# Kernel optimization log

Hardware: AMD Instinct MI355X
Metric: run time of the kernel (lower is better)

The kernel has to match this reference:

```python
import jax, jax.numpy as jnp
import numpy as np
import math

D_MODEL = 64
D_STATE = 16
IMG = 64
GROUPS = 4
EPS = 1e-5


def group_norm(x, gamma, beta):
    B, C, H, W = x.shape
    xg = x.reshape(B, GROUPS, C // GROUPS, H, W)
    mu = xg.mean(axis=(2, 3, 4), keepdims=True)
    var = ((xg - mu) ** 2).mean(axis=(2, 3, 4), keepdims=True)
    xn = ((xg - mu) * jax.lax.rsqrt(var + EPS)).reshape(B, C, H, W)
    return xn * gamma[None, :, None, None] + beta[None, :, None, None]


def circ_conv(x, w, b=None):
    # 3x3 conv with circular padding, NCHW/OIHW
    xp = jnp.pad(x, ((0, 0), (0, 0), (1, 1), (1, 1)), mode='wrap')
    y = jax.lax.conv_general_dilated(xp, w, window_strides=(1, 1), padding='VALID',
                                     dimension_numbers=('NCHW', 'OIHW', 'NCHW'))
    if b is not None:
        y = y + b[None, :, None, None]
    return y


def setup_inputs() -> dict:
    key = jax.random.key(0)
    ks = jax.random.split(key, 6)
    B = 4
    u_t = jax.random.normal(ks[0], (B, D_MODEL, IMG, IMG), dtype=jnp.float32)
    s_prev = jax.random.normal(ks[1], (B, 3, D_MODEL, D_STATE, IMG, IMG), dtype=jnp.float32)
    gamma = jnp.ones((D_MODEL,), jnp.float32)
    beta = jnp.zeros((D_MODEL,), jnp.float32)
    w_delta = jax.random.normal(ks[2], (D_MODEL, D_MODEL, 3, 3), jnp.float32) * 0.05
    b_delta = jnp.zeros((D_MODEL,), jnp.float32)
    w_B = jax.random.normal(ks[3], (D_STATE, D_MODEL, 3, 3), jnp.float32) * 0.05
    w_C = jax.random.normal(ks[4], (D_STATE, D_MODEL, 3, 3), jnp.float32) * 0.05
    log_A_real = jnp.full((D_MODEL, D_STATE), math.log(0.5), jnp.float32)
    D_param = jnp.ones((D_MODEL,), jnp.float32)
    dt_inv_softplus = jnp.asarray(math.log(math.e - 1.0), jnp.float32)
    return {'u_t': u_t, 's_prev': s_prev, 'gamma': gamma, 'beta': beta,
            'w_delta': w_delta, 'b_delta': b_delta, 'w_B': w_B, 'w_C': w_C,
            'log_A_real': log_A_real, 'D_param': D_param, 'dt_inv_softplus': dt_inv_softplus}


def reference(u_t, s_prev, gamma, beta, w_delta, b_delta, w_B, w_C, log_A_real, D_param, dt_inv_softplus):
    B, D, H, W = u_t.shape
    N = D_STATE
    un = group_norm(u_t, gamma, beta)
    delta = jax.nn.softplus(circ_conv(un, w_delta, b_delta) + dt_inv_softplus)
    delta = jnp.clip(delta, 1e-4, 5.0)                     # [B,D,H,W]
    B_val = circ_conv(un, w_B)                              # [B,N,H,W]
    C_val = circ_conv(un, w_C)                              # [B,N,H,W]
    A = -jnp.exp(log_A_real)                                # [D,N]
    delta_bc = delta[:, :, None]                            # [B,D,1,H,W]
    A_bar = jnp.exp(delta_bc * A[None, :, :, None, None])   # [B,D,N,H,W]
    B_bar = delta_bc * B_val[:, None]                       # [B,D,N,H,W]
    m0, mx, my = s_prev[:, 0], s_prev[:, 1], s_prev[:, 2]   # each [B,D,N,H,W]
    # spectral gradient of m0 over last two (spatial) axes
    ky_ = np.fft.fftfreq(H).astype(np.float32) * 2.0 * np.pi
    kx_ = np.fft.fftfreq(W).astype(np.float32) * 2.0 * np.pi
    ky, kx = jnp.meshgrid(jnp.asarray(ky_), jnp.asarray(kx_), indexing='ij')
    m0f = jnp.fft.fft2(m0)
    grad_y = jnp.fft.ifft2(m0f * (1j * ky)).real
    grad_x = jnp.fft.ifft2(m0f * (1j * kx)).real
    m0_new = A_bar * m0 + B_bar * u_t[:, :, None]
    mx_new = A_bar * (mx - grad_x)
    my_new = A_bar * (my - grad_y)
    s_new = jnp.stack([m0_new, mx_new, my_new], axis=1)     # [B,3,D,N,H,W]
    y_state = jnp.einsum('bdnhw,bnhw->bdhw', m0_new, C_val)
    y_new = (y_state + u_t * D_param[None, :, None, None])[:, None]  # [B,1,D,H,W]
    return (y_new, s_new)
```

## Files before the change

### kernel.cpp

```cpp
#include <hip/hip_runtime.h>
#include <hip/hip_bf16.h>

#define B_ 4
#define D_ 64
#define N_ 16
#define HW_ 4096

#define LDSA 72
#define LDSB 66
#define EXPU 68

#define OFF_D2    0u
#define OFF_ATAB  8192u
#define OFF_MEAN  12288u
#define OFF_RSTD  12352u
#define OFF_W9    16384u
#define OFF_UNT   131072u
#define OFF_DELTA 2228224u
#define OFF_BVAL  6422528u
#define OFF_CVAL  7471104u
#define OFF_YBUF  8519680u

typedef __bf16 v8bf __attribute__((ext_vector_type(8)));
typedef float  v4f  __attribute__((ext_vector_type(4)));

__device__ __forceinline__ unsigned short f2bf(float f){
  __hip_bfloat16 h = __float2bfloat16(f);
  return *reinterpret_cast<unsigned short*>(&h);
}
__device__ __forceinline__ float bf2f(unsigned int u){
  union{unsigned int i; float f;} c; c.i = (u & 0xffffu)<<16; return c.f;
}
__device__ __forceinline__ v8bf ld8bf(const unsigned short* p){
  union{uint4 u; v8bf v;} c; c.u = *(const uint4*)p; return c.v;
}

__device__ __forceinline__ void bar_lgkm(){
  asm volatile("s_waitcnt lgkmcnt(0)" ::: "memory");
  __builtin_amdgcn_s_barrier();
  __builtin_amdgcn_sched_barrier(0);
}

__global__ void k_init(const float* __restrict__ logA,
                       unsigned short* __restrict__ D2w, float* __restrict__ Atab){
  int g = blockIdx.x*256 + threadIdx.x;
  if(g < 4096){
    int r = g>>6, m = g&63;
    int p = (r - m) & 63;
    float s = 0.f;
    for(int k=1;k<32;k++) s += (float)k * sinf(0.09817477042468103f * (float)(k*p));
    D2w[g] = f2bf(-0.0030679615757712823f * s);
  } else if(g < 5120){
    int idx = g - 4096;
    Atab[idx] = -__expf(logA[idx]);
  }
}

__global__ void k_wrepack(const float* __restrict__ wd,
                          const float* __restrict__ wB,
                          const float* __restrict__ wC,
                          unsigned short* __restrict__ W9){
  int idx = blockIdx.x*256 + threadIdx.x;
  if(idx >= 96*64) return;
  int co = idx>>6, ci = idx&63;
  const float* src;
  if(co < 64)      src = wd + ((size_t)co*64 + ci)*9;
  else if(co < 80) src = wB + ((size_t)(co-64)*64 + ci)*9;
  else             src = wC + ((size_t)(co-80)*64 + ci)*9;
  for(int tap=0; tap<9; tap++)
    W9[((size_t)tap*96 + co)*64 + ci] = f2bf(src[tap]);
}

__global__ void k_gnstats(const float* __restrict__ u,
                          float* __restrict__ meanw, float* __restrict__ rstdw){
  int bg = blockIdx.x;
  const float* base = u + (size_t)bg*65536;
  int t = threadIdx.x;
  float s=0.f, s2=0.f;
  for(int j=0;j<16;j++){
    float4 v = ((const float4*)base)[t + 1024*j];
    s  += v.x+v.y+v.z+v.w;
    s2 += v.x*v.x+v.y*v.y+v.z*v.z+v.w*v.w;
  }
  for(int o=32;o>0;o>>=1){ s += __shfl_down(s,o); s2 += __shfl_down(s2,o); }
  __shared__ float ls[16], ls2[16];
  int wv = t>>6;
  if((t&63)==0){ ls[wv]=s; ls2[wv]=s2; }
  __syncthreads();
  if(t==0){
    float S=0.f,S2=0.f;
    for(int i=0;i<16;i++){ S+=ls[i]; S2+=ls2[i]; }
    float mu = S/65536.f;
    float var = S2/65536.f - mu*mu;
    meanw[bg]=mu; rstdw[bg]=rsqrtf(var+1e-5f);
  }
}

__global__ __launch_bounds__(256) void k_unT(
    const float* __restrict__ u_t,
    const float* __restrict__ meanw, const float* __restrict__ rstdw,
    const float* __restrict__ gamma, const float* __restrict__ beta,
    unsigned short* __restrict__ unT){
  __shared__ unsigned short T[64*LDSA];
  int bid = blockIdx.x;
  int b = bid>>6, h = bid&63;
  int t = threadIdx.x;
  int w = t&63, cg = t>>6;
  #pragma unroll
  for(int i=0;i<16;i++){
    int c = cg*16 + i;
    float x = u_t[(((size_t)b*64 + c)*64 + h)*64 + w];
    int g = c>>4;
    float v = (x - meanw[b*4+g])*rstdw[b*4+g]*gamma[c] + beta[c];
    T[w*LDSA + c] = f2bf(v);
  }
  __syncthreads();
  int w2 = t>>2, cq = t&3;
  uint4 v0 = *(uint4*)&T[w2*LDSA + cq*16];
  uint4 v1 = *(uint4*)&T[w2*LDSA + cq*16 + 8];
  uint4* dst = (uint4*)(unT + ((size_t)b*HW_ + h*64 + w2)*64 + cq*16);
  dst[0] = v0; dst[1] = v1;
}

__global__ __launch_bounds__(256) void k_conv(
    const unsigned short* __restrict__ unT,
    const unsigned short* __restrict__ W9,
    const float* __restrict__ b_d,
    const float* __restrict__ dtp,
    float* __restrict__ deltaw, float* __restrict__ Bvalw, float* __restrict__ Cvalw){
  int bid = blockIdx.x;
  int b = bid>>6, h = bid&63;
  int t = threadIdx.x;
  int wv = t>>6, l = t&63;
  int lr = l&15, lk = l>>4;
  v4f acc[6];
  #pragma unroll
  for(int i=0;i<6;i++) acc[i] = (v4f){0.f,0.f,0.f,0.f};
  int wpix = wv*16 + lr;
  #pragma unroll
  for(int tap=0; tap<9; tap++){
    int dy = tap/3 - 1, dx = tap - (tap/3)*3 - 1;
    int hh = (h+dy)&63;
    int ww = (wpix+dx)&63;
    const unsigned short* bp = unT + ((size_t)b*HW_ + hh*64 + ww)*64;
    const unsigned short* ap = W9 + (size_t)tap*96*64;
    #pragma unroll
    for(int ks=0; ks<2; ks++){
      int k0 = ks*32 + lk*8;
      v8bf bfrag = ld8bf(bp + k0);
      #pragma unroll
      for(int mt=0; mt<6; mt++){
        v8bf afrag = ld8bf(ap + (mt*16+lr)*64 + k0);
        acc[mt] = __builtin_amdgcn_mfma_f32_16x16x32_bf16(afrag, bfrag, acc[mt], 0,0,0);
      }
    }
  }
  float dt = dtp[0];
  int p = h*64 + wpix;
  #pragma unroll
  for(int mt=0; mt<6; mt++){
    #pragma unroll
    for(int r=0;r<4;r++){
      int co = mt*16 + lk*4 + r;
      float v = acc[mt][r];
      if(co < 64){
        float x = v + b_d[co] + dt;
        float sp = (x > 15.f) ? x : log1pf(__expf(x));
        sp = fminf(fmaxf(sp, 1e-4f), 5.f);
        deltaw[((size_t)b*64 + co)*HW_ + p] = sp;
      } else if(co < 80){
        Bvalw[((size_t)b*16 + (co-64))*HW_ + p] = v;
      } else {
        Cvalw[((size_t)b*16 + (co-80))*HW_ + p] = v;
      }
    }
  }
}

__global__ __launch_bounds__(256, 4) void k_main(
    const float* __restrict__ u_t,
    const float* __restrict__ s_prev,
    const unsigned short* __restrict__ D2w,
    const float* __restrict__ Atab,
    const float* __restrict__ deltaw,
    const float* __restrict__ Bvalw,
    const float* __restrict__ Cvalw,
    float* __restrict__ ybuf,
    float* __restrict__ out_s){
  __shared__ __align__(16) unsigned short Mbuf[64*LDSA + 64*LDSB];
  __shared__ __align__(16) unsigned short D2s[64*LDSA];
  unsigned short* Ms72 = Mbuf;
  unsigned short* Ms66 = Mbuf + 64*LDSA;
  unsigned short* EXx  = Mbuf;
  unsigned short* EXy  = Mbuf + 64*EXPU;

  int bid = blockIdx.x;
  int pair = bid & 255;
  int b = pair & 3, d = pair >> 2;
  int nq = bid >> 8;
  int t = threadIdx.x;
  int wv = t>>6, l = t&63;
  int lr = l & 15, lk = l >> 4;
  int r0 = wv*16;

  size_t bd = (size_t)b*64 + d;
  const size_t PL = (size_t)D_*N_*HW_;
  size_t sbase = (size_t)b*3*PL + (size_t)d*N_*HW_;
  int n0 = nq*4;

  const float* m0base = s_prev + sbase;
  const float* mxbase = s_prev + sbase + PL;
  const float* mybase = s_prev + sbase + 2*PL;

  int g0 = t, g1 = t+256, g2 = t+512, g3 = t+768;

  uint4 d2v0 = ((const uint4*)D2w)[t];
  uint4 d2v1 = ((const uint4*)D2w)[t+256];
  { int r = t>>3, cb = t&7;            *(uint4*)&D2s[r*LDSA + cb*8] = d2v0; }
  { int c2 = t+256; int r = c2>>3, cb = c2&7; *(uint4*)&D2s[r*LDSA + cb*8] = d2v1; }
  const float4* uv4 = (const float4*)(u_t + bd*HW_);
  const float4* dv4 = (const float4*)(deltaw + bd*HW_);
  float4 uq0 = uv4[g0], uq1 = uv4[g1], uq2 = uv4[g2], uq3 = uv4[g3];
  float4 dq0 = dv4[g0], dq1 = dv4[g1], dq2 = dv4[g2], dq3 = dv4[g3];

  float4 yq0 = make_float4(0.f,0.f,0.f,0.f);
  float4 yq1 = yq0, yq2 = yq0, yq3 = yq0;

  for(int ni=0; ni<4; ni++){
    int n = n0 + ni;
    const float4* m0v = (const float4*)(m0base + (size_t)n*HW_);
    float4 pm0 = m0v[g0], pm1 = m0v[g1], pm2 = m0v[g2], pm3 = m0v[g3];
    const float4* mxv = (const float4*)(mxbase + (size_t)n*HW_);
    const float4* myv = (const float4*)(mybase + (size_t)n*HW_);
    float4 sx0 = mxv[g0], sx1 = mxv[g1], sx2 = mxv[g2], sx3 = mxv[g3];
    float4 sy0 = myv[g0], sy1 = myv[g1], sy2 = myv[g2], sy3 = myv[g3];

    #pragma unroll
    for(int j=0;j<4;j++){
      float4 v = (j==0)?pm0:(j==1)?pm1:(j==2)?pm2:pm3;
      int g = t + 256*j;
      int r = g>>4, cb = g&15;
      unsigned int lo = (unsigned int)f2bf(v.x) | ((unsigned int)f2bf(v.y)<<16);
      unsigned int hi = (unsigned int)f2bf(v.z) | ((unsigned int)f2bf(v.w)<<16);
      unsigned int* d72 = (unsigned int*)&Ms72[r*LDSA + cb*4];
      d72[0]=lo; d72[1]=hi;
      unsigned int* d66 = (unsigned int*)&Ms66[r*LDSB + cb*4];
      d66[0]=lo; d66[1]=hi;
    }
    bar_lgkm();

    v4f gxa[4], gya[4];
    #pragma unroll
    for(int ct=0; ct<4; ct++){
      v4f gx = {0.f,0.f,0.f,0.f}, gy = {0.f,0.f,0.f,0.f};
      #pragma unroll
      for(int ks=0; ks<2; ks++){
        int k0 = ks*32 + lk*8;
        v8bf a_gx = ld8bf(&D2s[(ct*16+lr)*LDSA + k0]);
        v8bf b_gx = ld8bf(&Ms72[(r0+lr)*LDSA + k0]);
        gx = __builtin_amdgcn_mfma_f32_16x16x32_bf16(a_gx, b_gx, gx, 0,0,0);
        union { unsigned short s[8]; v8bf v; } ag;
        #pragma unroll
        for(int i=0;i<8;i++) ag.s[i] = Ms66[(k0+i)*LDSB + ct*16 + lr];
        v8bf b_gy = ld8bf(&D2s[(r0+lr)*LDSA + k0]);
        gy = __builtin_amdgcn_mfma_f32_16x16x32_bf16(ag.v, b_gy, gy, 0,0,0);
      }
      gxa[ct] = gx; gya[ct] = gy;
    }
    bar_lgkm();

    #pragma unroll
    for(int ct=0; ct<4; ct++){
      int eo = (r0+lr)*EXPU + (ct*4+lk)*4;
      unsigned int x0 = (unsigned int)f2bf(gxa[ct][0]) | ((unsigned int)f2bf(gxa[ct][1])<<16);
      unsigned int x1 = (unsigned int)f2bf(gxa[ct][2]) | ((unsigned int)f2bf(gxa[ct][3])<<16);
      *(uint2*)&EXx[eo] = make_uint2(x0,x1);
      unsigned int y0 = (unsigned int)f2bf(gya[ct][0]) | ((unsigned int)f2bf(gya[ct][1])<<16);
      unsigned int y1 = (unsigned int)f2bf(gya[ct][2]) | ((unsigned int)f2bf(gya[ct][3])<<16);
      *(uint2*)&EXy[eo] = make_uint2(y0,y1);
    }
    bar_lgkm();

    float An = Atab[d*16 + n];
    const float4* Bv  = (const float4*)(Bvalw + ((size_t)b*16 + n)*HW_);
    const float4* Cv  = (const float4*)(Cvalw + ((size_t)b*16 + n)*HW_);
    float* so = out_s + sbase + (size_t)n*HW_;
    float4* so0 = (float4*)so;
    float4* so1 = (float4*)(so + PL);
    float4* so2 = (float4*)(so + 2*PL);

    #pragma unroll
    for(int k=0; k<4; k++){
      int g = t + 256*k;
      float4 B4  = Bv[g];
      float4 C4  = Cv[g];
      int eo = (g>>4)*EXPU + (g&15)*4;
      uint2 ux = *(const uint2*)&EXx[eo];
      uint2 uy = *(const uint2*)&EXy[eo];
      float4 m04 = (k==0)?pm0:(k==1)?pm1:(k==2)?pm2:pm3;
      float4 mx4 = (k==0)?sx0:(k==1)?sx1:(k==2)?sx2:sx3;
      float4 my4 = (k==0)?sy0:(k==1)?sy1:(k==2)?sy2:sy3;
      float4 u4  = (k==0)?uq0:(k==1)?uq1:(k==2)?uq2:uq3;
      float4 dv_ = (k==0)?dq0:(k==1)?dq1:(k==2)?dq2:dq3;
      float4 ab, m0n, mxn, myn;
      ab.x = __expf(dv_.x*An);
      ab.y = __expf(dv_.y*An);
      ab.z = __expf(dv_.z*An);
      ab.w = __expf(dv_.w*An);
      m0n.x = ab.x*m04.x + dv_.x*B4.x*u4.x;
      m0n.y = ab.y*m04.y + dv_.y*B4.y*u4.y;
      m0n.z = ab.z*m04.z + dv_.z*B4.z*u4.z;
      m0n.w = ab.w*m04.w + dv_.w*B4.w*u4.w;
      mxn.x = ab.x*(mx4.x - bf2f(ux.x));
      mxn.y = ab.y*(mx4.y - bf2f(ux.x>>16));
      mxn.z = ab.z*(mx4.z - bf2f(ux.y));
      mxn.w = ab.w*(mx4.w - bf2f(ux.y>>16));
      myn.x = ab.x*(my4.x - bf2f(uy.x));
      myn.y = ab.y*(my4.y - bf2f(uy.x>>16));
      myn.z = ab.z*(my4.z - bf2f(uy.y));
      myn.w = ab.w*(my4.w - bf2f(uy.y>>16));
      if(k==0){ yq0.x += m0n.x*C4.x; yq0.y += m0n.y*C4.y; yq0.z += m0n.z*C4.z; yq0.w += m0n.w*C4.w; }
      if(k==1){ yq1.x += m0n.x*C4.x; yq1.y += m0n.y*C4.y; yq1.z += m0n.z*C4.z; yq1.w += m0n.w*C4.w; }
      if(k==2){ yq2.x += m0n.x*C4.x; yq2.y += m0n.y*C4.y; yq2.z += m0n.z*C4.z; yq2.w += m0n.w*C4.w; }
      if(k==3){ yq3.x += m0n.x*C4.x; yq3.y += m0n.y*C4.y; yq3.z += m0n.z*C4.z; yq3.w += m0n.w*C4.w; }
      so0[g] = m0n;
      so1[g] = mxn;
      so2[g] = myn;
    }
    __syncthreads();
  }

  float* yb = ybuf + bd*HW_;
  #pragma unroll
  for(int k=0; k<4; k++){
    int p = 4*(t + 256*k);
    float4 yv = (k==0)?yq0:(k==1)?yq1:(k==2)?yq2:yq3;
    atomicAdd(&yb[p+0], yv.x);
    atomicAdd(&yb[p+1], yv.y);
    atomicAdd(&yb[p+2], yv.z);
    atomicAdd(&yb[p+3], yv.w);
  }
}

__global__ void k_y(const float* __restrict__ ybuf,
                    const float* __restrict__ u_t,
                    const float* __restrict__ Dp,
                    float* __restrict__ out_y){
  int i = blockIdx.x*blockDim.x + threadIdx.x;
  int d = (i>>10)&63;
  float Dv = Dp[d];
  float4 uv = ((const float4*)u_t)[i];
  float4 yv = ((const float4*)ybuf)[i];
  float4 o;
  o.x = yv.x + uv.x*Dv;
  o.y = yv.y + uv.y*Dv;
  o.z = yv.z + uv.z*Dv;
  o.w = yv.w + uv.w*Dv;
  ((float4*)out_y)[i] = o;
}

extern "C" void kernel_launch(void* const* d_in, const int* in_sizes, int n_in,
                              void* d_out, int out_size, void* d_ws, size_t ws_size,
                              hipStream_t stream){
  const float* u_t    = (const float*)d_in[0];
  const float* s_prev = (const float*)d_in[1];
  const float* gamma  = (const float*)d_in[2];
  const float* beta   = (const float*)d_in[3];
  const float* w_d    = (const float*)d_in[4];
  const float* b_d    = (const float*)d_in[5];
  const float* w_B    = (const float*)d_in[6];
  const float* w_C    = (const float*)d_in[7];
  const float* logA   = (const float*)d_in[8];
  const float* Dp     = (const float*)d_in[9];
  const float* dtp    = (const float*)d_in[10];

  char* ws = (char*)d_ws;
  unsigned short* D2w  = (unsigned short*)(ws + OFF_D2);
  float* Atab          = (float*)(ws + OFF_ATAB);
  float* meanw         = (float*)(ws + OFF_MEAN);
  float* rstdw         = (float*)(ws + OFF_RSTD);
  unsigned short* W9   = (unsigned short*)(ws + OFF_W9);
  unsigned short* unT  = (unsigned short*)(ws + OFF_UNT);
  float* deltaw        = (float*)(ws + OFF_DELTA);
  float* Bvalw         = (float*)(ws + OFF_BVAL);
  float* Cvalw         = (float*)(ws + OFF_CVAL);
  float* ybuf          = (float*)(ws + OFF_YBUF);

  float* out_y = (float*)d_out;
  float* out_s = out_y + 1048576;

  hipMemsetAsync(ws + OFF_YBUF, 0, 4u*1048576u, stream);
  k_init   <<<20, 256, 0, stream>>>(logA, D2w, Atab);
  k_wrepack<<<24, 256, 0, stream>>>(w_d, w_B, w_C, W9);
  k_gnstats<<<16, 1024, 0, stream>>>(u_t, meanw, rstdw);
  k_unT    <<<256, 256, 0, stream>>>(u_t, meanw, rstdw, gamma, beta, unT);
  k_conv   <<<256, 256, 0, stream>>>(unT, W9, b_d, dtp, deltaw, Bvalw, Cvalw);
  k_main   <<<1024, 256, 0, stream>>>(u_t, s_prev, D2w, Atab, deltaw, Bvalw, Cvalw, ybuf, out_s);
  k_y      <<<1024, 256, 0, stream>>>(ybuf, u_t, Dp, out_y);
}
```

Baseline: 185.3 us.

## Remap k_main pixel ownership per wave to replace block barrier with wave wait

Reassigns which pixels each thread handles so that every wave owns a 16-row strip of the 64x64 plane for loading, the gradient MFMA output, and the elementwise update. Because each wave now reads back only the gradient rows it wrote itself, the second block-wide barrier is replaced by a per-wave lgkmcnt wait. The redundant LDSA-padded copy of m0 and the aliasing of the exchange buffers are removed, and D2 moves to the 66 stride. Separate LDS buffers for the exchange remove the write-after-read hazard, at the cost of more LDS per block and possibly more bank conflicts at the 66 stride.

```diff
diff --git a/kernel.cpp b/kernel.cpp
--- a/kernel.cpp
+++ b/kernel.cpp
@@ -38,6 +38,11 @@
 __device__ __forceinline__ void bar_lgkm(){
   asm volatile("s_waitcnt lgkmcnt(0)" ::: "memory");
   __builtin_amdgcn_s_barrier();
+  __builtin_amdgcn_sched_barrier(0);
+}
+
+__device__ __forceinline__ void wave_lgkm(){
+  asm volatile("s_waitcnt lgkmcnt(0)" ::: "memory");
   __builtin_amdgcn_sched_barrier(0);
 }
 
@@ -187,12 +192,10 @@
     const float* __restrict__ Cvalw,
     float* __restrict__ ybuf,
     float* __restrict__ out_s){
-  __shared__ __align__(16) unsigned short Mbuf[64*LDSA + 64*LDSB];
-  __shared__ __align__(16) unsigned short D2s[64*LDSA];
-  unsigned short* Ms72 = Mbuf;
-  unsigned short* Ms66 = Mbuf + 64*LDSA;
-  unsigned short* EXx  = Mbuf;
-  unsigned short* EXy  = Mbuf + 64*EXPU;
+  __shared__ __align__(16) unsigned short Ms66[64*LDSB];
+  __shared__ __align__(16) unsigned short D2s [64*LDSB];
+  __shared__ __align__(16) unsigned short EXx [64*EXPU];
+  __shared__ __align__(16) unsigned short EXy [64*EXPU];
 
   int bid = blockIdx.x;
   int pair = bid & 255;
@@ -202,6 +205,7 @@
   int wv = t>>6, l = t&63;
   int lr = l & 15, lk = l >> 4;
   int r0 = wv*16;
+  int gA = wv*256 + l;
 
   size_t bd = (size_t)b*64 + d;
   const size_t PL = (size_t)D_*N_*HW_;
@@ -212,16 +216,14 @@
   const float* mxbase = s_prev + sbase + PL;
   const float* mybase = s_prev + sbase + 2*PL;
 
-  int g0 = t, g1 = t+256, g2 = t+512, g3 = t+768;
-
   uint4 d2v0 = ((const uint4*)D2w)[t];
   uint4 d2v1 = ((const uint4*)D2w)[t+256];
-  { int r = t>>3, cb = t&7;            *(uint4*)&D2s[r*LDSA + cb*8] = d2v0; }
-  { int c2 = t+256; int r = c2>>3, cb = c2&7; *(uint4*)&D2s[r*LDSA + cb*8] = d2v1; }
+  { int r = t>>3, cb = t&7;            *(uint4*)&D2s[r*LDSB + cb*8] = d2v0; }
+  { int c2 = t+256; int r = c2>>3, cb = c2&7; *(uint4*)&D2s[r*LDSB + cb*8] = d2v1; }
   const float4* uv4 = (const float4*)(u_t + bd*HW_);
   const float4* dv4 = (const float4*)(deltaw + bd*HW_);
-  float4 uq0 = uv4[g0], uq1 = uv4[g1], uq2 = uv4[g2], uq3 = uv4[g3];
-  float4 dq0 = dv4[g0], dq1 = dv4[g1], dq2 = dv4[g2], dq3 = dv4[g3];
+  float4 uq0 = uv4[gA], uq1 = uv4[gA+64], uq2 = uv4[gA+128], uq3 = uv4[gA+192];
+  float4 dq0 = dv4[gA], dq1 = dv4[gA+64], dq2 = dv4[gA+128], dq3 = dv4[gA+192];
 
   float4 yq0 = make_float4(0.f,0.f,0.f,0.f);
   float4 yq1 = yq0, yq2 = yq0, yq3 = yq0;
@@ -229,57 +231,47 @@
   for(int ni=0; ni<4; ni++){
     int n = n0 + ni;
     const float4* m0v = (const float4*)(m0base + (size_t)n*HW_);
-    float4 pm0 = m0v[g0], pm1 = m0v[g1], pm2 = m0v[g2], pm3 = m0v[g3];
+    float4 pm0 = m0v[gA], pm1 = m0v[gA+64], pm2 = m0v[gA+128], pm3 = m0v[gA+192];
     const float4* mxv = (const float4*)(mxbase + (size_t)n*HW_);
     const float4* myv = (const float4*)(mybase + (size_t)n*HW_);
-    float4 sx0 = mxv[g0], sx1 = mxv[g1], sx2 = mxv[g2], sx3 = mxv[g3];
-    float4 sy0 = myv[g0], sy1 = myv[g1], sy2 = myv[g2], sy3 = myv[g3];
+    float4 sx0 = mxv[gA], sx1 = mxv[gA+64], sx2 = mxv[gA+128], sx3 = mxv[gA+192];
+    float4 sy0 = myv[gA], sy1 = myv[gA+64], sy2 = myv[gA+128], sy3 = myv[gA+192];
 
     #pragma unroll
     for(int j=0;j<4;j++){
       float4 v = (j==0)?pm0:(j==1)?pm1:(j==2)?pm2:pm3;
-      int g = t + 256*j;
-      int r = g>>4, cb = g&15;
+      int row = r0 + 4*j + lk;
       unsigned int lo = (unsigned int)f2bf(v.x) | ((unsigned int)f2bf(v.y)<<16);
       unsigned int hi = (unsigned int)f2bf(v.z) | ((unsigned int)f2bf(v.w)<<16);
-      unsigned int* d72 = (unsigned int*)&Ms72[r*LDSA + cb*4];
-      d72[0]=lo; d72[1]=hi;
-      unsigned int* d66 = (unsigned int*)&Ms66[r*LDSB + cb*4];
+      unsigned int* d66 = (unsigned int*)&Ms66[row*LDSB + lr*4];
       d66[0]=lo; d66[1]=hi;
     }
     bar_lgkm();
 
-    v4f gxa[4], gya[4];
     #pragma unroll
     for(int ct=0; ct<4; ct++){
       v4f gx = {0.f,0.f,0.f,0.f}, gy = {0.f,0.f,0.f,0.f};
       #pragma unroll
       for(int ks=0; ks<2; ks++){
         int k0 = ks*32 + lk*8;
-        v8bf a_gx = ld8bf(&D2s[(ct*16+lr)*LDSA + k0]);
-        v8bf b_gx = ld8bf(&Ms72[(r0+lr)*LDSA + k0]);
+        v8bf a_gx = ld8bf(&D2s[(ct*16+lr)*LDSB + k0]);
+        v8bf b_gx = ld8bf(&Ms66[(r0+lr)*LDSB + k0]);
         gx = __builtin_amdgcn_mfma_f32_16x16x32_bf16(a_gx, b_gx, gx, 0,0,0);
         union { unsigned short s[8]; v8bf v; } ag;
         #pragma unroll
         for(int i=0;i<8;i++) ag.s[i] = Ms66[(k0+i)*LDSB + ct*16 + lr];
-        v8bf b_gy = ld8bf(&D2s[(r0+lr)*LDSA + k0]);
+        v8bf b_gy = ld8bf(&D2s[(r0+lr)*LDSB + k0]);
         gy = __builtin_amdgcn_mfma_f32_16x16x32_bf16(ag.v, b_gy, gy, 0,0,0);
       }
-      gxa[ct] = gx; gya[ct] = gy;
-    }
-    bar_lgkm();
-
-    #pragma unroll
-    for(int ct=0; ct<4; ct++){
       int eo = (r0+lr)*EXPU + (ct*4+lk)*4;
-      unsigned int x0 = (unsigned int)f2bf(gxa[ct][0]) | ((unsigned int)f2bf(gxa[ct][1])<<16);
-      unsigned int x1 = (unsigned int)f2bf(gxa[ct][2]) | ((unsigned int)f2bf(gxa[ct][3])<<16);
+      unsigned int x0 = (unsigned int)f2bf(gx[0]) | ((unsigned int)f2bf(gx[1])<<16);
+      unsigned int x1 = (unsigned int)f2bf(gx[2]) | ((unsigned int)f2bf(gx[3])<<16);
       *(uint2*)&EXx[eo] = make_uint2(x0,x1);
-      unsigned int y0 = (unsigned int)f2bf(gya[ct][0]) | ((unsigned int)f2bf(gya[ct][1])<<16);
-      unsigned int y1 = (unsigned int)f2bf(gya[ct][2]) | ((unsigned int)f2bf(gya[ct][3])<<16);
+      unsigned int y0 = (unsigned int)f2bf(gy[0]) | ((unsigned int)f2bf(gy[1])<<16);
+      unsigned int y1 = (unsigned int)f2bf(gy[2]) | ((unsigned int)f2bf(gy[3])<<16);
       *(uint2*)&EXy[eo] = make_uint2(y0,y1);
     }
-    bar_lgkm();
+    wave_lgkm();
 
     float An = Atab[d*16 + n];
     const float4* Bv  = (const float4*)(Bvalw + ((size_t)b*16 + n)*HW_);
@@ -291,10 +283,10 @@
 
     #pragma unroll
     for(int k=0; k<4; k++){
-      int g = t + 256*k;
+      int g = gA + 64*k;
       float4 B4  = Bv[g];
       float4 C4  = Cv[g];
-      int eo = (g>>4)*EXPU + (g&15)*4;
+      int eo = (r0 + 4*k + lk)*EXPU + lr*4;
       uint2 ux = *(const uint2*)&EXx[eo];
       uint2 uy = *(const uint2*)&EXy[eo];
       float4 m04 = (k==0)?pm0:(k==1)?pm1:(k==2)?pm2:pm3;
@@ -333,7 +325,7 @@
   float* yb = ybuf + bd*HW_;
   #pragma unroll
   for(int k=0; k<4; k++){
-    int p = 4*(t + 256*k);
+    int p = 4*(gA + 64*k);
     float4 yv = (k==0)?yq0:(k==1)?yq1:(k==2)?yq2:yq3;
     atomicAdd(&yb[p+0], yv.x);
     atomicAdd(&yb[p+1], yv.y);
```

Measured after the change: 174.5 us. -5.8%, faster.
